# Optimization experiments

Measured on AMD Instinct MI355X. Metric: run time of the kernel, lower is better.

## Reference

```python
import jax, jax.numpy as jnp
import numpy as np

DIM = 64
HID = DIM // 8  # 8, hidden width of pos_fc / attn_fc
B, N, V = 1024, 64, 8
NUM_IDS = 10


def setup_inputs() -> dict:
    key = jax.random.key(0)
    ks = jax.random.split(key, 24)
    stdv = 1.0 / np.sqrt(DIM * DIM)
    inp = {
        "q": jax.random.normal(ks[0], (B, N, DIM), jnp.float32),
        "k": jax.random.normal(ks[1], (B, N, V, DIM), jnp.float32),
        "pos": jax.random.normal(ks[2], (B, N, V, 4), jnp.float32),
        "strength": jax.random.normal(ks[3], (512,), jnp.float32),
        # learned params
        "q_tbl": jax.random.uniform(ks[4], (NUM_IDS, DIM * DIM), jnp.float32, -stdv, stdv),
        "k_tbl": jax.random.uniform(ks[5], (NUM_IDS, DIM * DIM), jnp.float32, -stdv, stdv),
        "v_tbl": jax.random.uniform(ks[6], (NUM_IDS, DIM * DIM), jnp.float32, -stdv, stdv),
        "pos_w1": jax.random.normal(ks[7], (4, HID), jnp.float32) * 0.5,
        "pos_b1": jax.random.normal(ks[8], (HID,), jnp.float32) * 0.1,
        "pos_w2": jax.random.normal(ks[9], (HID, DIM), jnp.float32) * 0.2,
        "pos_b2": jax.random.normal(ks[10], (DIM,), jnp.float32) * 0.1,
        "attn_w1": jax.random.normal(ks[11], (DIM, HID), jnp.float32) * 0.1,
        "attn_b1": jax.random.normal(ks[12], (HID,), jnp.float32) * 0.1,
        "attn_w2": jax.random.normal(ks[13], (HID, DIM), jnp.float32) * 0.2,
        "attn_b2": jax.random.normal(ks[14], (DIM,), jnp.float32) * 0.1,
        "out_w": jax.random.normal(ks[15], (DIM, DIM), jnp.float32) * 0.1,
        "out_b": jax.random.normal(ks[16], (DIM,), jnp.float32) * 0.1,
        "str_w": jax.random.normal(ks[17], (512, DIM), jnp.float32) * 0.04,
        "str_b": jax.random.normal(ks[18], (DIM,), jnp.float32) * 0.1,
        # int args
        "mask": jax.random.randint(ks[19], (B, N, V, 1), 0, 2, jnp.int32),
        "embed_id1": 3,
    }
    return inp


def reference(q, k, pos, strength, q_tbl, k_tbl, v_tbl,
              pos_w1, pos_b1, pos_w2, pos_b2,
              attn_w1, attn_b1, attn_w2, attn_b2,
              out_w, out_b, str_w, str_b, mask, embed_id1):
    s = strength @ str_w + str_b                       # [DIM]
    Wq = q_tbl[embed_id1].reshape(DIM, DIM)
    Wk = k_tbl[embed_id1].reshape(DIM, DIM)
    Wv = v_tbl[embed_id1].reshape(DIM, DIM)
    # F.linear(x, W) = x @ W.T ; note v is computed from k (as in source)
    qh = q @ Wq.T + s                                  # [B,N,DIM]
    kh = k @ Wk.T + s                                  # [B,N,V,DIM]
    vh = k @ Wv.T + s                                  # [B,N,V,DIM]
    p = jax.nn.relu(pos @ pos_w1 + pos_b1) @ pos_w2 + pos_b2   # [B,N,V,DIM]
    attn = kh - qh[:, :, None, :] + p                  # [B,N,V,DIM]
    attn = jax.nn.relu(attn @ attn_w1 + attn_b1) @ attn_w2 + attn_b2
    attn = jnp.where(mask == 0, jnp.float32(-1e9), attn)
    attn = jax.nn.softmax(attn, axis=-2)               # softmax over views V
    x = ((vh + p) * attn).sum(axis=2)                  # [B,N,DIM]
    x = x @ out_w + out_b
    return x
```

## Files before the change

kernel.cpp:

```cpp
#include <hip/hip_runtime.h>

#define TBL 4096

#define WS_S    0
#define WS_AT   64
#define WS_BQT  576
#define WS_CT   1088
#define WS_C0   1152
#define WS_F32_END 1536
#define PB_AT   0
#define PB_BQN  512
#define PB_CT   1024
#define PB_W2T  1088
#define PB_PW2T 1600
#define PB_PW1  2112
#define PB_VT   2176
#define PB_OWT  6272
#define PB_END  10368

typedef __attribute__((ext_vector_type(8))) short bf16x8;
typedef __attribute__((ext_vector_type(4))) float f32x4;

__device__ inline short f2bf(float f) {
    union { float f; unsigned u; } v; v.f = f;
    unsigned r = v.u + 0x7fffu + ((v.u >> 16) & 1u);
    return (short)(r >> 16);
}

__device__ inline bf16x8 pack8(const float* x) {
    bf16x8 r;
    #pragma unroll
    for (int i = 0; i < 8; ++i) r[i] = f2bf(x[i]);
    return r;
}

__device__ inline bf16x8 loadpack(const float* p) {
    float4 a = *(const float4*)p;
    float4 b = *(const float4*)(p + 4);
    float t[8] = {a.x, a.y, a.z, a.w, b.x, b.y, b.z, b.w};
    return pack8(t);
}

__device__ inline bf16x8 pack8t(float4 a, float4 b) {
    union { unsigned u[4]; bf16x8 v; } r;
    r.u[0] = __builtin_amdgcn_perm(__float_as_uint(a.y), __float_as_uint(a.x), 0x07060302u);
    r.u[1] = __builtin_amdgcn_perm(__float_as_uint(a.w), __float_as_uint(a.z), 0x07060302u);
    r.u[2] = __builtin_amdgcn_perm(__float_as_uint(b.y), __float_as_uint(b.x), 0x07060302u);
    r.u[3] = __builtin_amdgcn_perm(__float_as_uint(b.w), __float_as_uint(b.z), 0x07060302u);
    return r.v;
}

__global__ __launch_bounds__(256) void precompute_kernel(
    const float* __restrict__ strength, const float* __restrict__ str_w,
    const float* __restrict__ str_b,
    const float* __restrict__ q_tbl, const float* __restrict__ k_tbl,
    const float* __restrict__ attn_w1, const float* __restrict__ attn_b1,
    const float* __restrict__ pos_w2, const float* __restrict__ pos_b2,
    const int* __restrict__ embed_id, float* __restrict__ ws)
{
    __shared__ float red[4][64];
    const int t = threadIdx.x;
    const int blk = blockIdx.x;
    const int id = embed_id[0];
    if (blk == 0) {
        const int d = t & 63, part = t >> 6;
        float acc = 0.f;
        for (int i = part * 128; i < part * 128 + 128; ++i)
            acc += strength[i] * str_w[i * 64 + d];
        red[part][d] = acc;
        __syncthreads();
        if (t < 64)
            ws[WS_S + t] = red[0][t] + red[1][t] + red[2][t] + red[3][t] + str_b[t];
    } else if (blk <= 2) {
        const int h = (blk - 1) * 4 + (t >> 6);
        const int j = t & 63;
        const float* W = k_tbl + (size_t)id * TBL;
        float acc = 0.f;
        for (int d = 0; d < 64; ++d) acc += W[d * 64 + j] * attn_w1[d * 8 + h];
        ws[WS_AT + h * 64 + j] = acc;
    } else if (blk <= 4) {
        const int h = (blk - 3) * 4 + (t >> 6);
        const int j = t & 63;
        const float* W = q_tbl + (size_t)id * TBL;
        float acc = 0.f;
        for (int d = 0; d < 64; ++d) acc += W[d * 64 + j] * attn_w1[d * 8 + h];
        ws[WS_BQT + h * 64 + j] = acc;
    } else {
        if (t < 64) {
            const int h = t >> 3, g = t & 7;
            float acc = 0.f;
            for (int d = 0; d < 64; ++d) acc += pos_w2[g * 64 + d] * attn_w1[d * 8 + h];
            ws[WS_CT + t] = acc;
        } else if (t < 72) {
            const int h = t - 64;
            float acc = attn_b1[h];
            for (int d = 0; d < 64; ++d) acc += pos_b2[d] * attn_w1[d * 8 + h];
            ws[WS_C0 + h] = acc;
        }
    }
}

__global__ __launch_bounds__(256) void pack_kernel(
    const float* __restrict__ v_tbl,
    const float* __restrict__ pos_w1, const float* __restrict__ pos_w2,
    const float* __restrict__ attn_w2, const float* __restrict__ out_w,
    const int* __restrict__ embed_id, float* __restrict__ ws)
{
    short* pk = (short*)(ws + WS_F32_END);
    const int i = blockIdx.x * 256 + threadIdx.x;
    if (i >= PB_END) return;
    const int id = embed_id[0];
    if (i < 512) {
        pk[i] = f2bf(ws[WS_AT + i]);
    } else if (i < 1024) {
        pk[i] = f2bf(-ws[WS_BQT + (i - 512)]);
    } else if (i < 1088) {
        pk[i] = f2bf(ws[WS_CT + (i - 1024)]);
    } else if (i < 1600) {
        const int idx = i - 1088, d = idx >> 3, h = idx & 7;
        pk[i] = f2bf(attn_w2[h * 64 + d]);
    } else if (i < 2112) {
        const int idx = i - 1600, d = idx >> 3, h = idx & 7;
        pk[i] = f2bf(pos_w2[h * 64 + d]);
    } else if (i < 2176) {
        const int idx = i - 2112, h = idx >> 3, j = idx & 7;
        pk[i] = (j < 4) ? f2bf(pos_w1[j * 8 + h]) : (short)0;
    } else if (i < 6272) {
        pk[i] = f2bf(v_tbl[(size_t)id * TBL + (i - 2176)]);
    } else {
        const int idx = i - 6272, e = idx >> 6, d = idx & 63;
        pk[i] = f2bf(out_w[d * 64 + e]);
    }
}

__global__ __launch_bounds__(256, 3) void attn2d_main(
    const float* __restrict__ q, const float* __restrict__ k,
    const float* __restrict__ pos,
    const float* __restrict__ pos_b1, const float* __restrict__ pos_b2,
    const float* __restrict__ attn_b2, const float* __restrict__ out_b,
    const int* __restrict__ mask,
    const float* __restrict__ ws, float* __restrict__ out)
{
    __shared__ __align__(16) short hp_bf[4][16 * 8];
    __shared__ __align__(16) short rh_bf[4][16 * 8];
    __shared__ __align__(16) float qB_lds[4][16 * 8];
    __shared__ __align__(16) short x_bf[4][16 * 72];

    const int tid  = threadIdx.x;
    const int lane = tid & 63;
    const int wiv  = __builtin_amdgcn_readfirstlane(tid >> 6);
    const int q4   = lane >> 4;
    const int col  = lane & 15;

    short* hp_w = hp_bf[wiv];
    short* rh_w = rh_bf[wiv];
    float* qB_w = qB_lds[wiv];
    short* x_w  = x_bf[wiv];

    const int wid = blockIdx.x * 4 + wiv;
    const short* pk = (const short*)(ws + WS_F32_END);
    const bf16x8 z{};

    bf16x8 Bv[4][2];
    #pragma unroll
    for (int t = 0; t < 4; ++t)
        #pragma unroll
        for (int c = 0; c < 2; ++c)
            Bv[t][c] = *(const bf16x8*)&pk[PB_VT + (t * 16 + col) * 64 + c * 32 + q4 * 8];
    bf16x8 Bh[2];
    #pragma unroll
    for (int c = 0; c < 2; ++c)
        Bh[c] = (col < 8) ? *(const bf16x8*)&pk[PB_AT + col * 64 + c * 32 + q4 * 8] : z;
    const bf16x8 Bct  = (q4 == 0 && col < 8) ? *(const bf16x8*)&pk[PB_CT + col * 8] : z;
    const bf16x8 Bpw1 = (q4 == 0 && col < 8) ? *(const bf16x8*)&pk[PB_PW1 + col * 8] : z;
    bf16x8 Bw2[4], Bpw2[4];
    #pragma unroll
    for (int t = 0; t < 4; ++t) {
        Bw2[t]  = (q4 == 0) ? *(const bf16x8*)&pk[PB_W2T  + (t * 16 + col) * 8] : z;
        Bpw2[t] = (q4 == 0) ? *(const bf16x8*)&pk[PB_PW2T + (t * 16 + col) * 8] : z;
    }

    float b2a4[4], sb4[4], ob4[4];
    #pragma unroll
    for (int t = 0; t < 4; ++t) {
        b2a4[t] = attn_b2[t * 16 + col];
        sb4[t]  = ws[WS_S + t * 16 + col] + pos_b2[t * 16 + col];
        ob4[t]  = out_b[t * 16 + col];
    }
    const float c0r = (col < 8) ? ws[WS_C0 + col] : 0.f;
    const float b1c = (col < 8) ? pos_b1[col] : 0.f;

    {
        bf16x8 Bq0 = (col < 8) ? *(const bf16x8*)&pk[PB_BQN + col * 64 + q4 * 8] : z;
        bf16x8 Bq1 = (col < 8) ? *(const bf16x8*)&pk[PB_BQN + col * 64 + 32 + q4 * 8] : z;
        bf16x8 Aq0 = loadpack(q + (size_t)(wid * 16 + col) * 64 + q4 * 8);
        bf16x8 Aq1 = loadpack(q + (size_t)(wid * 16 + col) * 64 + 32 + q4 * 8);
        f32x4 aq = {0.f, 0.f, 0.f, 0.f};
        aq = __builtin_amdgcn_mfma_f32_16x16x32_bf16(Aq0, Bq0, aq, 0, 0, 0);
        aq = __builtin_amdgcn_mfma_f32_16x16x32_bf16(Aq1, Bq1, aq, 0, 0, 0);
        if (col < 8) {
            #pragma unroll
            for (int r = 0; r < 4; ++r) qB_w[(q4 * 4 + r) * 8 + col] = aq[r];
        }
    }

    float4 kr[2][2][2]; float4 pr[2]; int4 mr[2];
    auto issue = [&](int b, int it2) {
        const size_t pair = (size_t)wid * 8 + it2;
        const float* kb = k + (pair * 16 + col) * 64 + q4 * 8;
        kr[b][0][0] = *(const float4*)kb;
        kr[b][0][1] = *(const float4*)(kb + 4);
        kr[b][1][0] = *(const float4*)(kb + 32);
        kr[b][1][1] = *(const float4*)(kb + 36);
        pr[b] = (q4 == 0) ? *(const float4*)(pos + (pair * 16 + col) * 4)
                          : make_float4(0.f, 0.f, 0.f, 0.f);
        mr[b] = *(const int4*)(mask + pair * 16 + q4 * 4);
    };
    issue(0, 0);

    #pragma unroll 2
    for (int it = 0; it < 8; ++it) {
        const int b = it & 1;
        if (it < 7) issue(b ^ 1, it + 1);
        const int rowbase = it * 2 + (q4 >> 1);

        bf16x8 Apos = z;
        if (q4 == 0) {
            float t4[8] = {pr[b].x, pr[b].y, pr[b].z, pr[b].w, 0.f, 0.f, 0.f, 0.f};
            Apos = pack8(t4);
        }
        f32x4 hpc = {0.f, 0.f, 0.f, 0.f};
        hpc = __builtin_amdgcn_mfma_f32_16x16x32_bf16(Apos, Bpw1, hpc, 0, 0, 0);
        if (col < 8) {
            #pragma unroll
            for (int r = 0; r < 4; ++r)
                hp_w[(q4 * 4 + r) * 8 + col] = f2bf(fmaxf(hpc[r] + b1c, 0.f));
        }

        bf16x8 Ak0 = pack8t(kr[b][0][0], kr[b][0][1]);
        bf16x8 Ak1 = pack8t(kr[b][1][0], kr[b][1][1]);

        bf16x8 Ahp = z;
        if (lane < 16) Ahp = *(const bf16x8*)&hp_w[lane * 8];

        const float qbc = (col < 8) ? qB_w[rowbase * 8 + col] : 0.f;
        f32x4 acch = {0.f, 0.f, 0.f, 0.f};
        acch = __builtin_amdgcn_mfma_f32_16x16x32_bf16(Ak0, Bh[0], acch, 0, 0, 0);
        acch = __builtin_amdgcn_mfma_f32_16x16x32_bf16(Ak1, Bh[1], acch, 0, 0, 0);
        acch = __builtin_amdgcn_mfma_f32_16x16x32_bf16(Ahp, Bct,  acch, 0, 0, 0);
        if (col < 8) {
            #pragma unroll
            for (int r = 0; r < 4; ++r)
                rh_w[(q4 * 4 + r) * 8 + col] = f2bf(fmaxf(acch[r] + qbc + c0r, 0.f));
        }
        bf16x8 Arh = z;
        if (lane < 16) Arh = *(const bf16x8*)&rh_w[lane * 8];

        #pragma unroll
        for (int t = 0; t < 4; ++t) {
            f32x4 av = {0.f, 0.f, 0.f, 0.f};
            av = __builtin_amdgcn_mfma_f32_16x16x32_bf16(Ak0, Bv[t][0], av, 0, 0, 0);
            av = __builtin_amdgcn_mfma_f32_16x16x32_bf16(Ak1, Bv[t][1], av, 0, 0, 0);
            av = __builtin_amdgcn_mfma_f32_16x16x32_bf16(Ahp, Bpw2[t],  av, 0, 0, 0);
            f32x4 al = {0.f, 0.f, 0.f, 0.f};
            al = __builtin_amdgcn_mfma_f32_16x16x32_bf16(Arh, Bw2[t], al, 0, 0, 0);

            float att[4];
            att[0] = mr[b].x ? (al[0] + b2a4[t]) : -1e9f;
            att[1] = mr[b].y ? (al[1] + b2a4[t]) : -1e9f;
            att[2] = mr[b].z ? (al[2] + b2a4[t]) : -1e9f;
            att[3] = mr[b].w ? (al[3] + b2a4[t]) : -1e9f;

            float mp = fmaxf(fmaxf(att[0], att[1]), fmaxf(att[2], att[3]));
            float mm = fmaxf(mp, __shfl_xor(mp, 16));
            float e0 = __expf(att[0] - mm), e1 = __expf(att[1] - mm);
            float e2 = __expf(att[2] - mm), e3 = __expf(att[3] - mm);
            float sp = e0 + e1 + e2 + e3;
            float ss = sp + __shfl_xor(sp, 16);
            float xp = e0 * (av[0] + sb4[t]) + e1 * (av[1] + sb4[t])
                     + e2 * (av[2] + sb4[t]) + e3 * (av[3] + sb4[t]);
            float x = (xp + __shfl_xor(xp, 16)) * __builtin_amdgcn_rcpf(ss);
            if ((q4 & 1) == 0)
                x_w[rowbase * 72 + t * 16 + col] = f2bf(x);
        }
    }

    bf16x8 Ax[2];
    #pragma unroll
    for (int c = 0; c < 2; ++c)
        Ax[c] = *(const bf16x8*)&x_w[col * 72 + c * 32 + q4 * 8];
    #pragma unroll
    for (int t = 0; t < 4; ++t) {
        bf16x8 Bo0 = *(const bf16x8*)&pk[PB_OWT + (t * 16 + col) * 64 + q4 * 8];
        bf16x8 Bo1 = *(const bf16x8*)&pk[PB_OWT + (t * 16 + col) * 64 + 32 + q4 * 8];
        f32x4 a = {0.f, 0.f, 0.f, 0.f};
        a = __builtin_amdgcn_mfma_f32_16x16x32_bf16(Ax[0], Bo0, a, 0, 0, 0);
        a = __builtin_amdgcn_mfma_f32_16x16x32_bf16(Ax[1], Bo1, a, 0, 0, 0);
        #pragma unroll
        for (int r = 0; r < 4; ++r)
            out[((size_t)wid * 16 + q4 * 4 + r) * 64 + t * 16 + col] = a[r] + ob4[t];
    }
}

extern "C" void kernel_launch(void* const* d_in, const int* in_sizes, int n_in,
                              void* d_out, int out_size, void* d_ws, size_t ws_size,
                              hipStream_t stream) {
    const float* q        = (const float*)d_in[0];
    const float* k        = (const float*)d_in[1];
    const float* pos      = (const float*)d_in[2];
    const float* strength = (const float*)d_in[3];
    const float* q_tbl    = (const float*)d_in[4];
    const float* k_tbl    = (const float*)d_in[5];
    const float* v_tbl    = (const float*)d_in[6];
    const float* pos_w1   = (const float*)d_in[7];
    const float* pos_b1   = (const float*)d_in[8];
    const float* pos_w2   = (const float*)d_in[9];
    const float* pos_b2   = (const float*)d_in[10];
    const float* attn_w1  = (const float*)d_in[11];
    const float* attn_b1  = (const float*)d_in[12];
    const float* attn_w2  = (const float*)d_in[13];
    const float* attn_b2  = (const float*)d_in[14];
    const float* out_w    = (const float*)d_in[15];
    const float* out_b    = (const float*)d_in[16];
    const float* str_w    = (const float*)d_in[17];
    const float* str_b    = (const float*)d_in[18];
    const int*   mask     = (const int*)d_in[19];
    const int*   embed    = (const int*)d_in[20];
    float* ws  = (float*)d_ws;
    float* out = (float*)d_out;

    hipLaunchKernelGGL(precompute_kernel, dim3(6), dim3(256), 0, stream,
                       strength, str_w, str_b, q_tbl, k_tbl, attn_w1, attn_b1,
                       pos_w2, pos_b2, embed, ws);
    hipLaunchKernelGGL(pack_kernel, dim3((PB_END + 255) / 256), dim3(256), 0, stream,
                       v_tbl, pos_w1, pos_w2, attn_w2, out_w, embed, ws);
    hipLaunchKernelGGL(attn2d_main, dim3(1024), dim3(256), 0, stream,
                       q, k, pos, pos_b1, pos_b2, attn_b2, out_b, mask, ws, out);
}
```

Before: 292.9 us.

## Halve per-wave work, double grid, compute pos hidden layer on VALU

Each wave now handles 8 query rows (4 pairs) instead of 16, and the grid doubles to 2048 blocks, which gives more waves to hide memory latency. The loop is restructured into two fully unrolled bodies that each process two pairs, interleaving their MFMAs for more instruction-level parallelism. The pos_fc first layer moves from an MFMA plus an LDS round-trip to scalar VALU FMAs, dropping the hp LDS buffer. In exchange, the q-projection and output MFMAs now leave half their rows unused, per-wave weight loads happen twice as often across the grid, and register pressure rises.

```diff
diff --git a/kernel.cpp b/kernel.cpp
--- a/kernel.cpp
+++ b/kernel.cpp
@@ -136,15 +136,15 @@
 __global__ __launch_bounds__(256, 3) void attn2d_main(
     const float* __restrict__ q, const float* __restrict__ k,
     const float* __restrict__ pos,
-    const float* __restrict__ pos_b1, const float* __restrict__ pos_b2,
+    const float* __restrict__ pos_w1, const float* __restrict__ pos_b1,
+    const float* __restrict__ pos_b2,
     const float* __restrict__ attn_b2, const float* __restrict__ out_b,
     const int* __restrict__ mask,
     const float* __restrict__ ws, float* __restrict__ out)
 {
-    __shared__ __align__(16) short hp_bf[4][16 * 8];
-    __shared__ __align__(16) short rh_bf[4][16 * 8];
-    __shared__ __align__(16) float qB_lds[4][16 * 8];
-    __shared__ __align__(16) short x_bf[4][16 * 72];
+    __shared__ __align__(16) short rh_bf[4][2][16 * 8];
+    __shared__ __align__(16) float qB_lds[4][8 * 8];
+    __shared__ __align__(16) short x_bf[4][8 * 72];
 
     const int tid  = threadIdx.x;
     const int lane = tid & 63;
@@ -152,8 +152,6 @@
     const int q4   = lane >> 4;
     const int col  = lane & 15;
 
-    short* hp_w = hp_bf[wiv];
-    short* rh_w = rh_bf[wiv];
     float* qB_w = qB_lds[wiv];
     short* x_w  = x_bf[wiv];
 
@@ -171,14 +169,21 @@
     #pragma unroll
     for (int c = 0; c < 2; ++c)
         Bh[c] = (col < 8) ? *(const bf16x8*)&pk[PB_AT + col * 64 + c * 32 + q4 * 8] : z;
-    const bf16x8 Bct  = (q4 == 0 && col < 8) ? *(const bf16x8*)&pk[PB_CT + col * 8] : z;
-    const bf16x8 Bpw1 = (q4 == 0 && col < 8) ? *(const bf16x8*)&pk[PB_PW1 + col * 8] : z;
+    const bf16x8 Bct = (q4 == 0 && col < 8) ? *(const bf16x8*)&pk[PB_CT + col * 8] : z;
     bf16x8 Bw2[4], Bpw2[4];
     #pragma unroll
     for (int t = 0; t < 4; ++t) {
         Bw2[t]  = (q4 == 0) ? *(const bf16x8*)&pk[PB_W2T  + (t * 16 + col) * 8] : z;
         Bpw2[t] = (q4 == 0) ? *(const bf16x8*)&pk[PB_PW2T + (t * 16 + col) * 8] : z;
     }
+
+    float w1s[4][8], b1s[8];
+    #pragma unroll
+    for (int j = 0; j < 4; ++j)
+        #pragma unroll
+        for (int g = 0; g < 8; ++g) w1s[j][g] = pos_w1[j * 8 + g];
+    #pragma unroll
+    for (int g = 0; g < 8; ++g) b1s[g] = pos_b1[g];
 
     float b2a4[4], sb4[4], ob4[4];
     #pragma unroll
@@ -188,107 +193,122 @@
         ob4[t]  = out_b[t * 16 + col];
     }
     const float c0r = (col < 8) ? ws[WS_C0 + col] : 0.f;
-    const float b1c = (col < 8) ? pos_b1[col] : 0.f;
 
     {
         bf16x8 Bq0 = (col < 8) ? *(const bf16x8*)&pk[PB_BQN + col * 64 + q4 * 8] : z;
         bf16x8 Bq1 = (col < 8) ? *(const bf16x8*)&pk[PB_BQN + col * 64 + 32 + q4 * 8] : z;
-        bf16x8 Aq0 = loadpack(q + (size_t)(wid * 16 + col) * 64 + q4 * 8);
-        bf16x8 Aq1 = loadpack(q + (size_t)(wid * 16 + col) * 64 + 32 + q4 * 8);
+        bf16x8 Aq0 = loadpack(q + (size_t)(wid * 8 + (col & 7)) * 64 + q4 * 8);
+        bf16x8 Aq1 = loadpack(q + (size_t)(wid * 8 + (col & 7)) * 64 + 32 + q4 * 8);
         f32x4 aq = {0.f, 0.f, 0.f, 0.f};
         aq = __builtin_amdgcn_mfma_f32_16x16x32_bf16(Aq0, Bq0, aq, 0, 0, 0);
         aq = __builtin_amdgcn_mfma_f32_16x16x32_bf16(Aq1, Bq1, aq, 0, 0, 0);
-        if (col < 8) {
+        if (col < 8 && q4 < 2) {
             #pragma unroll
             for (int r = 0; r < 4; ++r) qB_w[(q4 * 4 + r) * 8 + col] = aq[r];
         }
     }
 
-    float4 kr[2][2][2]; float4 pr[2]; int4 mr[2];
-    auto issue = [&](int b, int it2) {
-        const size_t pair = (size_t)wid * 8 + it2;
-        const float* kb = k + (pair * 16 + col) * 64 + q4 * 8;
-        kr[b][0][0] = *(const float4*)kb;
-        kr[b][0][1] = *(const float4*)(kb + 4);
-        kr[b][1][0] = *(const float4*)(kb + 32);
-        kr[b][1][1] = *(const float4*)(kb + 36);
-        pr[b] = (q4 == 0) ? *(const float4*)(pos + (pair * 16 + col) * 4)
-                          : make_float4(0.f, 0.f, 0.f, 0.f);
-        mr[b] = *(const int4*)(mask + pair * 16 + q4 * 4);
+    float4 kf[2][2][2][2]; float4 pf[2][2]; int4 mf[2][2];
+    auto issue = [&](int buf, int body) {
+        #pragma unroll
+        for (int s = 0; s < 2; ++s) {
+            const size_t pair = (size_t)wid * 4 + body * 2 + s;
+            const float* kb = k + (pair * 16 + col) * 64 + q4 * 8;
+            kf[buf][s][0][0] = *(const float4*)kb;
+            kf[buf][s][0][1] = *(const float4*)(kb + 4);
+            kf[buf][s][1][0] = *(const float4*)(kb + 32);
+            kf[buf][s][1][1] = *(const float4*)(kb + 36);
+            pf[buf][s] = *(const float4*)(pos + (pair * 16 + col) * 4);
+            mf[buf][s] = *(const int4*)(mask + pair * 16 + q4 * 4);
+        }
     };
     issue(0, 0);
 
-    #pragma unroll 2
-    for (int it = 0; it < 8; ++it) {
-        const int b = it & 1;
-        if (it < 7) issue(b ^ 1, it + 1);
-        const int rowbase = it * 2 + (q4 >> 1);
-
-        bf16x8 Apos = z;
-        if (q4 == 0) {
-            float t4[8] = {pr[b].x, pr[b].y, pr[b].z, pr[b].w, 0.f, 0.f, 0.f, 0.f};
-            Apos = pack8(t4);
-        }
-        f32x4 hpc = {0.f, 0.f, 0.f, 0.f};
-        hpc = __builtin_amdgcn_mfma_f32_16x16x32_bf16(Apos, Bpw1, hpc, 0, 0, 0);
-        if (col < 8) {
+    #pragma unroll
+    for (int body = 0; body < 2; ++body) {
+        const int buf = body & 1;
+        if (body == 0) issue(1, 1);
+
+        bf16x8 Ak0[2], Ak1[2], Ahp[2];
+        float hv[2][8];
+        #pragma unroll
+        for (int s = 0; s < 2; ++s) {
+            Ak0[s] = pack8t(kf[buf][s][0][0], kf[buf][s][0][1]);
+            Ak1[s] = pack8t(kf[buf][s][1][0], kf[buf][s][1][1]);
+            const float4 pp = pf[buf][s];
             #pragma unroll
-            for (int r = 0; r < 4; ++r)
-                hp_w[(q4 * 4 + r) * 8 + col] = f2bf(fmaxf(hpc[r] + b1c, 0.f));
-        }
-
-        bf16x8 Ak0 = pack8t(kr[b][0][0], kr[b][0][1]);
-        bf16x8 Ak1 = pack8t(kr[b][1][0], kr[b][1][1]);
-
-        bf16x8 Ahp = z;
-        if (lane < 16) Ahp = *(const bf16x8*)&hp_w[lane * 8];
-
-        const float qbc = (col < 8) ? qB_w[rowbase * 8 + col] : 0.f;
-        f32x4 acch = {0.f, 0.f, 0.f, 0.f};
-        acch = __builtin_amdgcn_mfma_f32_16x16x32_bf16(Ak0, Bh[0], acch, 0, 0, 0);
-        acch = __builtin_amdgcn_mfma_f32_16x16x32_bf16(Ak1, Bh[1], acch, 0, 0, 0);
-        acch = __builtin_amdgcn_mfma_f32_16x16x32_bf16(Ahp, Bct,  acch, 0, 0, 0);
-        if (col < 8) {
+            for (int g = 0; g < 8; ++g)
+                hv[s][g] = fmaxf(b1s[g] + pp.x * w1s[0][g] + pp.y * w1s[1][g]
+                                        + pp.z * w1s[2][g] + pp.w * w1s[3][g], 0.f);
+            Ahp[s] = (q4 == 0) ? pack8(hv[s]) : z;
+        }
+
+        f32x4 acch[2];
+        #pragma unroll
+        for (int s = 0; s < 2; ++s) {
+            f32x4 a = {0.f, 0.f, 0.f, 0.f};
+            a = __builtin_amdgcn_mfma_f32_16x16x32_bf16(Ak0[s], Bh[0], a, 0, 0, 0);
+            a = __builtin_amdgcn_mfma_f32_16x16x32_bf16(Ak1[s], Bh[1], a, 0, 0, 0);
+            a = __builtin_amdgcn_mfma_f32_16x16x32_bf16(Ahp[s], Bct,  a, 0, 0, 0);
+            acch[s] = a;
+        }
+        #pragma unroll
+        for (int s = 0; s < 2; ++s) {
+            const int wlbn = (body * 2 + s) * 2 + (q4 >> 1);
+            const float qbc = (col < 8) ? qB_w[wlbn * 8 + col] : 0.f;
+            if (col < 8) {
+                #pragma unroll
+                for (int r = 0; r < 4; ++r)
+                    rh_bf[wiv][s][(q4 * 4 + r) * 8 + col] =
+                        f2bf(fmaxf(acch[s][r] + qbc + c0r, 0.f));
+            }
+        }
+        bf16x8 Arh[2];
+        #pragma unroll
+        for (int s = 0; s < 2; ++s)
+            Arh[s] = (lane < 16) ? *(const bf16x8*)&rh_bf[wiv][s][lane * 8] : z;
+
+        #pragma unroll
+        for (int t = 0; t < 4; ++t) {
+            f32x4 av[2], al[2];
             #pragma unroll
-            for (int r = 0; r < 4; ++r)
-                rh_w[(q4 * 4 + r) * 8 + col] = f2bf(fmaxf(acch[r] + qbc + c0r, 0.f));
-        }
-        bf16x8 Arh = z;
-        if (lane < 16) Arh = *(const bf16x8*)&rh_w[lane * 8];
-
-        #pragma unroll
-        for (int t = 0; t < 4; ++t) {
-            f32x4 av = {0.f, 0.f, 0.f, 0.f};
-            av = __builtin_amdgcn_mfma_f32_16x16x32_bf16(Ak0, Bv[t][0], av, 0, 0, 0);
-            av = __builtin_amdgcn_mfma_f32_16x16x32_bf16(Ak1, Bv[t][1], av, 0, 0, 0);
-            av = __builtin_amdgcn_mfma_f32_16x16x32_bf16(Ahp, Bpw2[t],  av, 0, 0, 0);
-            f32x4 al = {0.f, 0.f, 0.f, 0.f};
-            al = __builtin_amdgcn_mfma_f32_16x16x32_bf16(Arh, Bw2[t], al, 0, 0, 0);
-
-            float att[4];
-            att[0] = mr[b].x ? (al[0] + b2a4[t]) : -1e9f;
-            att[1] = mr[b].y ? (al[1] + b2a4[t]) : -1e9f;
-            att[2] = mr[b].z ? (al[2] + b2a4[t]) : -1e9f;
-            att[3] = mr[b].w ? (al[3] + b2a4[t]) : -1e9f;
-
-            float mp = fmaxf(fmaxf(att[0], att[1]), fmaxf(att[2], att[3]));
-            float mm = fmaxf(mp, __shfl_xor(mp, 16));
-            float e0 = __expf(att[0] - mm), e1 = __expf(att[1] - mm);
-            float e2 = __expf(att[2] - mm), e3 = __expf(att[3] - mm);
-            float sp = e0 + e1 + e2 + e3;
-            float ss = sp + __shfl_xor(sp, 16);
-            float xp = e0 * (av[0] + sb4[t]) + e1 * (av[1] + sb4[t])
-                     + e2 * (av[2] + sb4[t]) + e3 * (av[3] + sb4[t]);
-            float x = (xp + __shfl_xor(xp, 16)) * __builtin_amdgcn_rcpf(ss);
-            if ((q4 & 1) == 0)
-                x_w[rowbase * 72 + t * 16 + col] = f2bf(x);
+            for (int s = 0; s < 2; ++s) {
+                f32x4 a = {0.f, 0.f, 0.f, 0.f};
+                a = __builtin_amdgcn_mfma_f32_16x16x32_bf16(Ak0[s], Bv[t][0], a, 0, 0, 0);
+                a = __builtin_amdgcn_mfma_f32_16x16x32_bf16(Ak1[s], Bv[t][1], a, 0, 0, 0);
+                a = __builtin_amdgcn_mfma_f32_16x16x32_bf16(Ahp[s], Bpw2[t],  a, 0, 0, 0);
+                av[s] = a;
+                f32x4 l = {0.f, 0.f, 0.f, 0.f};
+                al[s] = __builtin_amdgcn_mfma_f32_16x16x32_bf16(Arh[s], Bw2[t], l, 0, 0, 0);
+            }
+            #pragma unroll
+            for (int s = 0; s < 2; ++s) {
+                const int4 mk = mf[buf][s];
+                float att[4];
+                att[0] = mk.x ? (al[s][0] + b2a4[t]) : -1e9f;
+                att[1] = mk.y ? (al[s][1] + b2a4[t]) : -1e9f;
+                att[2] = mk.z ? (al[s][2] + b2a4[t]) : -1e9f;
+                att[3] = mk.w ? (al[s][3] + b2a4[t]) : -1e9f;
+                float mp = fmaxf(fmaxf(att[0], att[1]), fmaxf(att[2], att[3]));
+                float mm = fmaxf(mp, __shfl_xor(mp, 16));
+                float e0 = __expf(att[0] - mm), e1 = __expf(att[1] - mm);
+                float e2 = __expf(att[2] - mm), e3 = __expf(att[3] - mm);
+                float sp = e0 + e1 + e2 + e3;
+                float ss = sp + __shfl_xor(sp, 16);
+                float xp = e0 * (av[s][0] + sb4[t]) + e1 * (av[s][1] + sb4[t])
+                         + e2 * (av[s][2] + sb4[t]) + e3 * (av[s][3] + sb4[t]);
+                float x = (xp + __shfl_xor(xp, 16)) * __builtin_amdgcn_rcpf(ss);
+                const int wlbn = (body * 2 + s) * 2 + (q4 >> 1);
+                if ((q4 & 1) == 0)
+                    x_w[wlbn * 72 + t * 16 + col] = f2bf(x);
+            }
         }
     }
 
     bf16x8 Ax[2];
     #pragma unroll
     for (int c = 0; c < 2; ++c)
-        Ax[c] = *(const bf16x8*)&x_w[col * 72 + c * 32 + q4 * 8];
+        Ax[c] = (col < 8) ? *(const bf16x8*)&x_w[col * 72 + c * 32 + q4 * 8] : z;
     #pragma unroll
     for (int t = 0; t < 4; ++t) {
         bf16x8 Bo0 = *(const bf16x8*)&pk[PB_OWT + (t * 16 + col) * 64 + q4 * 8];
@@ -297,8 +317,11 @@
         a = __builtin_amdgcn_mfma_f32_16x16x32_bf16(Ax[0], Bo0, a, 0, 0, 0);
         a = __builtin_amdgcn_mfma_f32_16x16x32_bf16(Ax[1], Bo1, a, 0, 0, 0);
         #pragma unroll
-        for (int r = 0; r < 4; ++r)
-            out[((size_t)wid * 16 + q4 * 4 + r) * 64 + t * 16 + col] = a[r] + ob4[t];
+        for (int r = 0; r < 4; ++r) {
+            const int row = q4 * 4 + r;
+            if (row < 8)
+                out[((size_t)wid * 8 + row) * 64 + t * 16 + col] = a[r] + ob4[t];
+        }
     }
 }
 
@@ -334,6 +357,6 @@
                        pos_w2, pos_b2, embed, ws);
     hipLaunchKernelGGL(pack_kernel, dim3((PB_END + 255) / 256), dim3(256), 0, stream,
                        v_tbl, pos_w1, pos_w2, attn_w2, out_w, embed, ws);
-    hipLaunchKernelGGL(attn2d_main, dim3(1024), dim3(256), 0, stream,
-                       q, k, pos, pos_b1, pos_b2, attn_b2, out_b, mask, ws, out);
-}
+    hipLaunchKernelGGL(attn2d_main, dim3(2048), dim3(256), 0, stream,
+                       q, k, pos, pos_w1, pos_b1, pos_b2, attn_b2, out_b, mask, ws, out);
+}
```

Result: slower. 323.5 us (+10.5%).
